# Performance work log

Measured on AMD Instinct MI355X. Metric: run time of the kernel, lower is better.

## Reference

```python
import math
import jax, jax.numpy as jnp
import numpy as np

Q_CLUSTER = 128
K_CLUSTER = 128


def _gaussian_orthogonal(m, d, rng):
    # gaussian_orthogonal_random_matrix with scaling=0 (row norms of fresh gaussians)
    blocks = []
    for _ in range(int(np.ceil(m / d))):
        g = rng.standard_normal((d, d))
        q, _ = np.linalg.qr(g)
        blocks.append(q.T)
    mat = np.concatenate(blocks, 0)[:m]
    norms = np.linalg.norm(rng.standard_normal((m, d)), axis=-1)
    return (mat * norms[:, None]).astype(np.float32)


def setup_inputs() -> dict:
    k = jax.random.key(0)
    kq, kk, kv = jax.random.split(k, 3)
    B, T, H, E = 2, 4096, 8, 64
    M, NH = 256, 4
    rng = np.random.default_rng(0)
    query = jax.random.normal(kq, (B, T, H, E), dtype=jnp.float32)
    key = jax.random.normal(kk, (B, T, H, E), dtype=jnp.float32)
    value = jax.random.normal(kv, (B, T, H, E), dtype=jnp.float32)
    proj = jnp.asarray(_gaussian_orthogonal(M, E, rng))
    alpha = jnp.asarray(rng.standard_normal((E + 2, NH)).astype(np.float32))
    beta = jnp.asarray(rng.uniform(0.0, 1.0, (1, NH)).astype(np.float32))
    return {"query": query, "key": key, "value": value, "proj": proj,
            "alpha": alpha, "beta": beta}


def _sort_to_buckets(x, perm, bucketsz):
    # x: (bh, s, d), perm: (nh, bh, s) -> (nh, bh, nbuckets, bucketsz, d)
    nh, bh, s = perm.shape
    g = jnp.take_along_axis(jnp.broadcast_to(x[None], (nh,) + x.shape),
                            perm[..., None], axis=2)
    return g.reshape(nh, bh, s // bucketsz, bucketsz, x.shape[-1])


def _unsort_from_buckets(s_x, perm_inv):
    nh, bh, nb, bsz, d = s_x.shape
    return jnp.take_along_axis(s_x.reshape(nh, bh, nb * bsz, d),
                               perm_inv[..., None], axis=2)


def _smyrf_forward(query, key, value, proj, alpha, beta):
    B, T, H, E = query.shape
    D = value.shape[-1]
    n_hashes = alpha.shape[-1]
    temp = 1.0 / math.sqrt(E)  # softmax_temp
    q = query.transpose(0, 2, 1, 3).reshape(B * H, T, E)
    k = key.transpose(0, 2, 1, 3).reshape(B * H, T, E)
    v = value.transpose(0, 2, 1, 3).reshape(B * H, T, D)

    # ---- XBOX+ asymmetric transform + E2LSH hashing (no grad path) ----
    qn = jnp.linalg.norm(q, axis=-1, keepdims=True)
    kn = jnp.linalg.norm(k, axis=-1, keepdims=True)
    MQ = jnp.max(qn, axis=1, keepdims=True)
    MK = jnp.max(kn, axis=1, keepdims=True)
    ext_q = jnp.sqrt(jnp.maximum(MQ ** 2 + MK ** 2 - qn ** 2, 0.0))
    ext_k = jnp.sqrt(jnp.maximum(MQ ** 2 + MK ** 2 - kn ** 2, 0.0))
    q_t = jnp.concatenate([q, ext_q, jnp.zeros_like(ext_q)], axis=-1)
    k_t = jnp.concatenate([k, jnp.zeros_like(ext_k), ext_k], axis=-1)
    q_hash = (q_t @ alpha + beta).transpose(2, 0, 1)  # (nh, bh, T)
    k_hash = (k_t @ alpha + beta).transpose(2, 0, 1)
    q_pos = jnp.argsort(q_hash, axis=-1)
    k_pos = jnp.argsort(k_hash, axis=-1)

    # ---- Performer (FAVOR+) softmax-kernel features with log scales ----
    dn = math.sqrt(temp)
    ratio = proj.shape[0] ** -0.5

    def feats(x, is_query):
        dash = jnp.einsum('bsd,md->bsm', dn * x, proj)
        diag = 0.5 * (dn ** 2) * jnp.sum(x * x, axis=-1, keepdims=True)
        logv = dash - diag
        if is_query:
            stab = jax.lax.stop_gradient(jnp.max(logv, axis=-1, keepdims=True))
        else:
            stab = jax.lax.stop_gradient(jnp.max(logv, axis=(-2, -1), keepdims=True))
        return jnp.exp(logv - stab) * ratio, stab

    q_prime, q_ls = feats(q, True)   # (bh, T, m), (bh, T, 1)
    k_prime, k_ls = feats(k, False)  # (bh, S, m), (bh, 1, 1)
    prime_log_scale = q_ls + k_ls    # (bh, T, 1)

    qk1 = jnp.einsum('btm,bm->bt', q_prime, k_prime.sum(axis=1))
    kv = jnp.einsum('bsm,bsd->bmd', k_prime, v)
    qkv = jnp.einsum('btm,bmd->btd', q_prime, kv)

    # ---- sort into LSH buckets, per-bucket attention ----
    s_q = _sort_to_buckets(q, q_pos, Q_CLUSTER)
    s_k = _sort_to_buckets(k, k_pos, K_CLUSTER)
    s_v = _sort_to_buckets(v, k_pos, K_CLUSTER)
    sq_p = _sort_to_buckets(q_prime, q_pos, Q_CLUSTER)
    sk_p = _sort_to_buckets(k_prime, k_pos, K_CLUSTER)
    s_pls = _sort_to_buckets(prime_log_scale, q_pos, Q_CLUSTER)

    inner = jnp.einsum('hbnie,hbnje->hbnij', s_q, s_k) * temp
    dots_prime = jnp.einsum('hbnim,hbnjm->hbnij', sq_p, sk_p)

    q_rev = jnp.argsort(q_pos, axis=-1)
    if n_hashes > 1:
        k_rev = jnp.argsort(k_pos, axis=-1)
        q_bidx = (q_rev // Q_CLUSTER).transpose(1, 2, 0)  # (bh, T, nh)
        k_bidx = (k_rev // K_CLUSTER).transpose(1, 2, 0)
        s_qb = _sort_to_buckets(q_bidx, q_pos, Q_CLUSTER)
        s_kb = _sort_to_buckets(k_bidx, k_pos, K_CLUSTER)
        dup = jnp.sum(s_qb[..., :, None, :] == s_kb[..., None, :, :],
                      axis=-1).astype(inner.dtype)
        inner = inner - jnp.log(dup)
        dots_prime = dots_prime / dup

    lse = jnp.maximum(jnp.max(inner, axis=-1, keepdims=True), s_pls)
    dots = jnp.exp(inner - lse) - dots_prime * jnp.exp(s_pls - lse)
    dots_sum = jnp.sum(dots, axis=-1, keepdims=True)
    so = jnp.einsum('hbnij,hbnjd->hbnid', dots, s_v)

    o = _unsort_from_buckets(so, q_rev)
    logits = _unsort_from_buckets(lse, q_rev)
    dots_sum_u = _unsort_from_buckets(dots_sum, q_rev)

    norm_ls = jax.nn.logsumexp(logits, axis=0)        # (bh, T, 1)
    probs = jnp.exp(logits - norm_ls[None])
    out_lsh = jnp.sum(o * probs, axis=0)
    prime_scale = jnp.exp(prime_log_scale - norm_ls)
    out = out_lsh + qkv * prime_scale
    normalization = jnp.sum(dots_sum_u * probs, axis=0) + qk1[..., None] * prime_scale
    out_n = out / jnp.maximum(normalization, 1e-6)
    return out_n.reshape(B, H, T, D).transpose(0, 2, 1, 3)


def reference(query, key, value, proj, alpha, beta):
    return _smyrf_forward(query, key, value, proj, alpha, beta)
```

## Files before the change

### kernel.cpp

```cpp
#include <hip/hip_runtime.h>
#include <stdint.h>
#include <math.h>

#define DEVI __device__ __forceinline__

constexpr int TB  = 2;
constexpr int TT  = 4096;
constexpr int TH  = 8;
constexpr int TE  = 64;
constexpr int TBH = 16;
constexpr int TM  = 256;
constexpr int TNH = 4;
constexpr float C_TEMP  = 0.125f;
constexpr float C_DN    = 0.35355339059327373f;
constexpr float C_RATIO = 0.0625f;

typedef __attribute__((ext_vector_type(8))) short bf16x8;
typedef __attribute__((ext_vector_type(4))) float f32x4;

constexpr size_t algn(size_t x){ return (x + 255) & ~(size_t)255; }
constexpr size_t OFF_QN2F = 0;
constexpr size_t OFF_KN2F = algn(OFF_QN2F + (size_t)TBH*TT*4);
constexpr size_t OFF_QN2D = algn(OFF_KN2F + (size_t)TBH*TT*4);
constexpr size_t OFF_KN2D = algn(OFF_QN2D + (size_t)TBH*TT*8);
constexpr size_t OFF_MQK2 = algn(OFF_KN2D + (size_t)TBH*TT*8);
constexpr size_t OFF_QMAXP= algn(OFF_MQK2 + (size_t)TBH*8);
constexpr size_t OFF_KMAXP= algn(OFF_QMAXP+ (size_t)TBH*16*8);
constexpr size_t OFF_QH   = algn(OFF_KMAXP+ (size_t)TBH*16*8);
constexpr size_t OFF_KH   = algn(OFF_QH   + (size_t)TNH*TBH*TT*8);
constexpr size_t OFF_QPOS = algn(OFF_KH   + (size_t)TNH*TBH*TT*8);
constexpr size_t OFF_KPOS = algn(OFF_QPOS + (size_t)TNH*TBH*TT*4);
constexpr size_t OFF_QREV = algn(OFF_KPOS + (size_t)TNH*TBH*TT*4);
constexpr size_t OFF_KREV = algn(OFF_QREV + (size_t)TNH*TBH*TT*4);
constexpr size_t OFF_KLSP = algn(OFF_KREV + (size_t)TNH*TBH*TT*4);
constexpr size_t OFF_KLS  = algn(OFF_KLSP + (size_t)TBH*128*4);
constexpr size_t OFF_QP   = algn(OFF_KLS  + (size_t)TBH*4);
constexpr size_t OFF_KP   = algn(OFF_QP   + (size_t)TBH*TT*TM*4);
constexpr size_t OFF_PLS  = algn(OFF_KP   + (size_t)TBH*TT*TM*4);
constexpr size_t OFF_KSUM = algn(OFF_PLS  + (size_t)TBH*TT*4);
constexpr size_t OFF_KV   = algn(OFF_KSUM + (size_t)TBH*TM*4);
constexpr size_t OFF_OT   = algn(OFF_KV   + (size_t)TBH*TM*TE*4);
constexpr size_t OFF_LSET = algn(OFF_OT   + (size_t)TNH*TBH*TT*TE*4);
constexpr size_t OFF_DSUM = algn(OFF_LSET + (size_t)TNH*TBH*TT*4);
constexpr size_t WS_NEED  = algn(OFF_DSUM + (size_t)TNH*TBH*TT*4);
constexpr size_t OFF_KVP  = OFF_QN2D;
constexpr size_t OFF_KSP  = OFF_KVP + (size_t)4*16*256*64*4;

DEVI float bf2f(uint32_t u16){ uint32_t x = u16 << 16; return __builtin_bit_cast(float, x); }
DEVI uint16_t f2bf(float f){
  uint32_t x = __builtin_bit_cast(uint32_t, f);
  uint32_t r = x + 0x7fffu + ((x >> 16) & 1u);
  return (uint16_t)(r >> 16);
}
DEVI int dupc(uint32_t x){
  return (int)((x & 0xffu) == 0) + (int)(((x >> 8) & 0xffu) == 0)
       + (int)(((x >> 16) & 0xffu) == 0) + (int)((x >> 24) == 0);
}
DEVI float lndup(int d){
  return d == 1 ? 0.f : d == 2 ? 0.69314718f : d == 3 ? 1.09861229f : 1.38629436f;
}
DEVI float rcpdup(int d){
  return d == 1 ? 1.f : d == 2 ? 0.5f : d == 3 ? 0.333333343f : 0.25f;
}

DEVI void stage64(char* rowp, const float4* src8, int hf){
  #pragma unroll
  for(int x = 0; x < 8; x++){
    float4 vv = src8[x];
    uint16_t hx = f2bf(vv.x), hy = f2bf(vv.y), hz = f2bf(vv.z), hw = f2bf(vv.w);
    float lx = vv.x - bf2f(hx), ly = vv.y - bf2f(hy), lz = vv.z - bf2f(hz), lw = vv.w - bf2f(hw);
    uint2 hp = make_uint2((uint32_t)hx | ((uint32_t)hy << 16), (uint32_t)hz | ((uint32_t)hw << 16));
    uint2 lp = make_uint2((uint32_t)f2bf(lx) | ((uint32_t)f2bf(ly) << 16),
                          (uint32_t)f2bf(lz) | ((uint32_t)f2bf(lw) << 16));
    *((uint2*)(rowp + 64*hf + 8*x)) = hp;
    *((uint2*)(rowp + 128 + 64*hf + 8*x)) = lp;
  }
}

__global__ void k_norms2(const float* __restrict__ q, const float* __restrict__ kk,
                         float* __restrict__ qn2f, float* __restrict__ kn2f,
                         double* __restrict__ qn2d, double* __restrict__ kn2d,
                         double* __restrict__ qmaxp, double* __restrict__ kmaxp){
  __shared__ double red[256];
  int bx = blockIdx.x; int chunk = bx & 15, bh = bx >> 4;
  int tid = threadIdx.x;
  int b = bh >> 3, hh = bh & 7;
  int t = chunk*256 + tid;
  const float4* r1 = (const float4*)(q + (((size_t)(b*TT + t)*TH) + hh)*TE);
  double s = 0.0;
  #pragma unroll
  for(int x = 0; x < 16; x++){
    float4 vv = r1[x];
    s += (double)vv.x*vv.x + (double)vv.y*vv.y + (double)vv.z*vv.z + (double)vv.w*vv.w;
  }
  qn2d[bh*TT + t] = s; qn2f[bh*TT + t] = (float)s;
  const float4* r2 = (const float4*)(kk + (((size_t)(b*TT + t)*TH) + hh)*TE);
  double s2 = 0.0;
  #pragma unroll
  for(int x = 0; x < 16; x++){
    float4 vv = r2[x];
    s2 += (double)vv.x*vv.x + (double)vv.y*vv.y + (double)vv.z*vv.z + (double)vv.w*vv.w;
  }
  kn2d[bh*TT + t] = s2; kn2f[bh*TT + t] = (float)s2;
  red[tid] = s; __syncthreads();
  for(int o = 128; o > 0; o >>= 1){ if(tid < o) red[tid] = fmax(red[tid], red[tid+o]); __syncthreads(); }
  if(tid == 0) qmaxp[bh*16 + chunk] = red[0];
  __syncthreads();
  red[tid] = s2; __syncthreads();
  for(int o = 128; o > 0; o >>= 1){ if(tid < o) red[tid] = fmax(red[tid], red[tid+o]); __syncthreads(); }
  if(tid == 0) kmaxp[bh*16 + chunk] = red[0];
}

__global__ void k_mqk(const double* __restrict__ qmaxp, const double* __restrict__ kmaxp,
                      double* __restrict__ mqk2){
  int bh = blockIdx.x;
  if(threadIdx.x == 0){
    double mq = -1e300, mk = -1e300;
    for(int i = 0; i < 16; i++){ mq = fmax(mq, qmaxp[bh*16 + i]); mk = fmax(mk, kmaxp[bh*16 + i]); }
    mqk2[bh] = mq + mk;
  }
}

__global__ void k_hash(const float* __restrict__ q, const float* __restrict__ kk,
                       const float* __restrict__ alpha, const float* __restrict__ beta,
                       const double* __restrict__ qn2d, const double* __restrict__ kn2d,
                       const double* __restrict__ mqk2,
                       double* __restrict__ qh, double* __restrict__ kh){
  __shared__ double al[264];
  __shared__ double be[4];
  int tid = threadIdx.x;
  for(int i = tid; i < 264; i += 256) al[i] = (double)alpha[i];
  if(tid < 4) be[tid] = (double)beta[tid];
  __syncthreads();
  int gid = blockIdx.x*256 + tid;
  int side = gid >> 16; int r = gid & 65535;
  int bh = r >> 12, t = r & 4095;
  int b = bh >> 3, hh = bh & 7;
  const float* x = (side ? kk : q) + (((size_t)(b*TT + t)*TH) + hh)*TE;
  const float4* xr = (const float4*)x;
  double a0 = 0.0, a1 = 0.0, a2 = 0.0, a3 = 0.0;
  #pragma unroll
  for(int c = 0; c < 16; c++){
    float4 vv = xr[c];
    const double* a = al + c*16;
    a0 += (double)vv.x*a[0]  + (double)vv.y*a[4]  + (double)vv.z*a[8]  + (double)vv.w*a[12];
    a1 += (double)vv.x*a[1]  + (double)vv.y*a[5]  + (double)vv.z*a[9]  + (double)vv.w*a[13];
    a2 += (double)vv.x*a[2]  + (double)vv.y*a[6]  + (double)vv.z*a[10] + (double)vv.w*a[14];
    a3 += (double)vv.x*a[3]  + (double)vv.y*a[7]  + (double)vv.z*a[11] + (double)vv.w*a[15];
  }
  double n2  = (side ? kn2d : qn2d)[bh*TT + t];
  double ext = sqrt(fmax(mqk2[bh] - n2, 0.0));
  int ec = side ? 65 : 64;
  double* dst = side ? kh : qh;
  dst[((size_t)0*TBH + bh)*TT + t] = a0 + ext*al[ec*4 + 0] + be[0];
  dst[((size_t)1*TBH + bh)*TT + t] = a1 + ext*al[ec*4 + 1] + be[1];
  dst[((size_t)2*TBH + bh)*TT + t] = a2 + ext*al[ec*4 + 2] + be[2];
  dst[((size_t)3*TBH + bh)*TT + t] = a3 + ext*al[ec*4 + 3] + be[3];
}

__global__ void k_sort(const double* __restrict__ qh, const double* __restrict__ kh,
                       int* __restrict__ qpos, int* __restrict__ kpos,
                       int* __restrict__ qrev, int* __restrict__ krev){
  __shared__ double v[4096];
  __shared__ int    ix[4096];
  int blk = blockIdx.x; int side = blk >> 6; int hb = blk & 63;
  const double* src = (side ? kh : qh) + (size_t)hb*TT;
  int tid = threadIdx.x;
  for(int i = tid; i < 4096; i += 1024){ v[i] = src[i]; ix[i] = i; }
  __syncthreads();
  for(int k = 2; k <= 4096; k <<= 1){
    for(int j = k >> 1; j > 0; j >>= 1){
      for(int i = tid; i < 4096; i += 1024){
        int l = i ^ j;
        if(l > i){
          double va = v[i], vb = v[l]; int ia = ix[i], ib = ix[l];
          bool gt  = (va > vb) || (va == vb && ia > ib);
          bool asc = ((i & k) == 0);
          if(gt == asc){ v[i] = vb; v[l] = va; ix[i] = ib; ix[l] = ia; }
        }
      }
      __syncthreads();
    }
  }
  int* pos = (side ? kpos : qpos) + (size_t)hb*TT;
  int* rev = (side ? krev : qrev) + (size_t)hb*TT;
  for(int i = tid; i < 4096; i += 1024){ int id = ix[i]; pos[i] = id; rev[id] = i; }
}

__launch_bounds__(512, 1)
__global__ void k_dash(const float* __restrict__ q, const float* __restrict__ kk,
                       const float* __restrict__ proj,
                       const float* __restrict__ qn2f, const float* __restrict__ kn2f,
                       float* __restrict__ qp, float* __restrict__ kdash,
                       float* __restrict__ klsp, float* __restrict__ pls){
  __shared__ __align__(16) float pjL[64*260];
  __shared__ __align__(16) float x_l[128*68];
  __shared__ float x_n[128];
  __shared__ float wred8[8];
  int tid = threadIdx.x;
  int bx = blockIdx.x;
  int side = bx >> 9; int r = bx & 511; int bh = r >> 5; int ch = r & 31;
  int b = bh >> 3, hh = bh & 7, t0 = ch*128;
  const float* x  = side ? kk   : q;
  const float* n2 = side ? kn2f : qn2f;

  #pragma unroll 8
  for(int it = 0; it < 32; it++){
    int idx = it*512 + tid;
    pjL[(idx & 63)*260 + (idx >> 6)] = proj[idx];
  }
  {
    int rr = tid >> 2, c = tid & 3;
    const float4* src = (const float4*)(x + (((size_t)(b*TT + t0 + rr)*TH) + hh)*TE);
    float4* dst = (float4*)(x_l + rr*68);
    #pragma unroll
    for(int i = 0; i < 4; i++) dst[c*4 + i] = src[c*4 + i];
  }
  if(tid < 128) x_n[tid] = n2[bh*TT + t0 + tid];
  __syncthreads();

  int ml = (tid & 15)*4;
  int tb = tid >> 4;
  float4 acc[4][4];
  #pragma unroll
  for(int tt = 0; tt < 4; tt++)
    #pragma unroll
    for(int g = 0; g < 4; g++) acc[tt][g] = make_float4(0.f,0.f,0.f,0.f);

  #pragma unroll 4
  for(int k4 = 0; k4 < 16; k4++){
    float4 xv[4];
    #pragma unroll
    for(int tt = 0; tt < 4; tt++)
      xv[tt] = *((const float4*)(x_l + (tb + 32*tt)*68 + k4*4));
    #pragma unroll
    for(int kk4 = 0; kk4 < 4; kk4++){
      int krow = k4*4 + kk4;
      #pragma unroll
      for(int g = 0; g < 4; g++){
        float4 pv = *((const float4*)(pjL + krow*260 + ml + 64*g));
        #pragma unroll
        for(int tt = 0; tt < 4; tt++){
          float xs = (kk4 == 0) ? xv[tt].x : (kk4 == 1) ? xv[tt].y : (kk4 == 2) ? xv[tt].z : xv[tt].w;
          acc[tt][g].x = fmaf(xs, pv.x, acc[tt][g].x);
          acc[tt][g].y = fmaf(xs, pv.y, acc[tt][g].y);
          acc[tt][g].z = fmaf(xs, pv.z, acc[tt][g].z);
          acc[tt][g].w = fmaf(xs, pv.w, acc[tt][g].w);
        }
      }
    }
  }

  if(side == 0){
    #pragma unroll
    for(int tt = 0; tt < 4; tt++){
      int t_r = tb + 32*tt;
      float diag = 0.5f*C_TEMP*x_n[t_r];
      float dd[4][4];
      float mx = -1e30f;
      #pragma unroll
      for(int g = 0; g < 4; g++){
        float4 a = acc[tt][g];
        dd[g][0] = fmaf(C_DN, a.x, -diag); dd[g][1] = fmaf(C_DN, a.y, -diag);
        dd[g][2] = fmaf(C_DN, a.z, -diag); dd[g][3] = fmaf(C_DN, a.w, -diag);
        mx = fmaxf(mx, fmaxf(fmaxf(dd[g][0], dd[g][1]), fmaxf(dd[g][2], dd[g][3])));
      }
      #pragma unroll
      for(int s = 1; s < 16; s <<= 1) mx = fmaxf(mx, __shfl_xor(mx, s, 64));
      size_t rowbase = ((size_t)bh*TT + t0 + t_r)*256;
      #pragma unroll
      for(int g = 0; g < 4; g++){
        float4 e;
        e.x = __expf(dd[g][0] - mx)*C_RATIO; e.y = __expf(dd[g][1] - mx)*C_RATIO;
        e.z = __expf(dd[g][2] - mx)*C_RATIO; e.w = __expf(dd[g][3] - mx)*C_RATIO;
        *((float4*)(qp + rowbase + ml + 64*g)) = e;
      }
      if((tid & 15) == 0) pls[(size_t)bh*TT + t0 + t_r] = mx;
    }
  } else {
    float mx = -1e30f;
    #pragma unroll
    for(int tt = 0; tt < 4; tt++){
      int t_r = tb + 32*tt;
      float diag = 0.5f*C_TEMP*x_n[t_r];
      size_t rowbase = ((size_t)bh*TT + t0 + t_r)*256;
      #pragma unroll
      for(int g = 0; g < 4; g++){
        float4 a = acc[tt][g];
        float4 dd;
        dd.x = fmaf(C_DN, a.x, -diag); dd.y = fmaf(C_DN, a.y, -diag);
        dd.z = fmaf(C_DN, a.z, -diag); dd.w = fmaf(C_DN, a.w, -diag);
        *((float4*)(kdash + rowbase + ml + 64*g)) = dd;
        mx = fmaxf(mx, fmaxf(fmaxf(dd.x, dd.y), fmaxf(dd.z, dd.w)));
      }
    }
    #pragma unroll
    for(int s = 32; s > 0; s >>= 1) mx = fmaxf(mx, __shfl_xor(mx, s, 64));
    if((tid & 63) == 0) wred8[tid >> 6] = mx;
    __syncthreads();
    if(tid == 0){
      float m = wred8[0];
      #pragma unroll
      for(int i = 1; i < 8; i++) m = fmaxf(m, wred8[i]);
      klsp[bh*32 + ch] = m;
    }
  }
}

__global__ void k_klsred(const float* __restrict__ klsp, float* __restrict__ kls){
  int bh = blockIdx.x, tid = threadIdx.x;
  float v = (tid < 32) ? klsp[bh*32 + tid] : -1e30f;
  #pragma unroll
  for(int o = 16; o > 0; o >>= 1) v = fmaxf(v, __shfl_xor(v, o, 64));
  if(tid == 0) kls[bh] = v;
}

__global__ void k_expk(float* __restrict__ kp, const float* __restrict__ kls){
  int tid = threadIdx.x; int blk = blockIdx.x;
  float4* p = (float4*)kp;
  size_t base = (size_t)blk*2048;
  float stab = kls[blk >> 7];
  #pragma unroll
  for(int i = 0; i < 8; i++){
    size_t ix = base + i*256 + tid;
    float4 vv = p[ix];
    vv.x = __expf(vv.x - stab)*C_RATIO; vv.y = __expf(vv.y - stab)*C_RATIO;
    vv.z = __expf(vv.z - stab)*C_RATIO; vv.w = __expf(vv.w - stab)*C_RATIO;
    p[ix] = vv;
  }
}

__global__ void k_kv2(const float* __restrict__ kp, const float* __restrict__ v,
                      float* __restrict__ kvp, float* __restrict__ ksump){
  int bx = blockIdx.x; int sc = bx >> 7; int rem = bx & 127; int bh = rem >> 3; int mt = rem & 7;
  int tid = threadIdx.x; int g = tid >> 6, d = tid & 63;
  int b = bh >> 3, hh = bh & 7; int m0 = mt*32;
  float a[8], sa[8];
  #pragma unroll
  for(int j = 0; j < 8; j++){ a[j] = 0.f; sa[j] = 0.f; }
  const float* kpb = kp + (size_t)bh*TT*256 + m0 + g;
  const float* vb  = v + (size_t)b*TT*TH*TE + hh*TE + d;
  int s0 = sc*1024;
  #pragma unroll 4
  for(int s = s0; s < s0 + 1024; s++){
    float vv = vb[(size_t)s*512];
    const float* kr = kpb + (size_t)s*256;
    #pragma unroll
    for(int j = 0; j < 8; j++){
      float kj = kr[4*j];
      a[j] = fmaf(kj, vv, a[j]); sa[j] += kj;
    }
  }
  #pragma unroll
  for(int j = 0; j < 8; j++){
    int m = m0 + g + 4*j;
    kvp[(((size_t)sc*16 + bh)*256 + m)*64 + d] = a[j];
    if(d == 0) ksump[((size_t)sc*16 + bh)*256 + m] = sa[j];
  }
}

__global__ void k_kvred(const float* __restrict__ kvp, const float* __restrict__ ksump,
                        float* __restrict__ kv, float* __restrict__ ksum){
  int bx = blockIdx.x, tid = threadIdx.x;
  if(bx < 256){
    size_t i = (size_t)bx*1024 + tid*4;
    float4 s = make_float4(0.f,0.f,0.f,0.f);
    #pragma unroll
    for(int sc = 0; sc < 4; sc++){
      float4 p = *((const float4*)(kvp + (size_t)sc*262144 + i));
      s.x += p.x; s.y += p.y; s.z += p.z; s.w += p.w;
    }
    *((float4*)(kv + i)) = s;
  } else {
    for(int m = tid; m < 4096; m += 256){
      float s = 0.f;
      #pragma unroll
      for(int sc = 0; sc < 4; sc++) s += ksump[sc*4096 + m];
      ksum[m] = s;
    }
  }
}

__launch_bounds__(256, 2)
__global__ void k_bucket(const float* __restrict__ q, const float* __restrict__ kk, const float* __restrict__ v,
                         const float* __restrict__ qp, const float* __restrict__ kp,
                         const int* __restrict__ qpos, const int* __restrict__ kpos,
                         const int* __restrict__ qrev, const int* __restrict__ krev,
                         const float* __restrict__ pls, const float* __restrict__ kls,
                         const float* __restrict__ qn2f, const float* __restrict__ kn2f,
                         float* __restrict__ o_t, float* __restrict__ lse_t, float* __restrict__ dsum_t){
  __shared__ __align__(16) char smem[73232];
  constexpr int OFS_B = 34816;
  int* qidxL   = (int*)(smem + 69632);
  int* kidxL   = (int*)(smem + 70144);
  int* qbpL    = (int*)(smem + 70656);
  int* kbpL    = (int*)(smem + 71168);
  float* lseL  = (float*)(smem + 71680);
  float* pfacL = (float*)(smem + 72192);
  float* kn2L  = (float*)(smem + 72704);
  float* kmaxP = (float*)(smem + 73216);

  int tid = threadIdx.x;
  int w = tid >> 6, lane = tid & 63, l15 = lane & 15, quad = lane >> 4;
  int bx = blockIdx.x; int n = bx & 31, bh = (bx >> 5) & 15, h = bx >> 9;
  int b = bh >> 3, hh = bh & 7;

  if(tid < 128){
    int tk = kpos[((size_t)h*TBH + bh)*TT + n*128 + tid];
    kidxL[tid] = tk;
    int pk = 0;
    #pragma unroll
    for(int h3 = 0; h3 < 4; h3++){ int rv = krev[((size_t)h3*TBH + bh)*TT + tk]; pk |= (rv >> 7) << (8*h3); }
    kbpL[tid] = pk;
    kn2L[tid] = kn2f[(size_t)bh*TT + tk];
    int tq = qpos[((size_t)h*TBH + bh)*TT + n*128 + tid];
    qidxL[tid] = tq;
    int pq = 0;
    #pragma unroll
    for(int h3 = 0; h3 < 4; h3++){ int rv = qrev[((size_t)h3*TBH + bh)*TT + tq]; pq |= (rv >> 7) << (8*h3); }
    qbpL[tid] = pq;
  }
  __syncthreads();
  if(tid < 64){
    float m = fmaxf(kn2L[tid], kn2L[tid + 64]);
    #pragma unroll
    for(int o = 32; o > 0; o >>= 1) m = fmaxf(m, __shfl_xor(m, o, 64));
    if(tid == 0) kmaxP[0] = m;
  }
  {
    int r = tid >> 1, hf = tid & 1;
    const float4* qs = (const float4*)(q  + (((size_t)(b*TT + qidxL[r])*TH) + hh)*TE) + hf*8;
    const float4* ks = (const float4*)(kk + (((size_t)(b*TT + kidxL[r])*TH) + hh)*TE) + hf*8;
    stage64(smem + r*272, qs, hf);
    stage64(smem + OFS_B + r*272, ks, hf);
  }
  __syncthreads();
  if(tid < 128){
    int tq = qidxL[tid];
    float plsv = pls[(size_t)bh*TT + tq] + kls[bh];
    float lse = fmaxf(plsv, C_TEMP * sqrtf(qn2f[(size_t)bh*TT + tq] * kmaxP[0]));
    lseL[tid] = lse;
    pfacL[tid] = __expf(plsv - lse);
  }

  f32x4 acc_s[2][8], acc_p[2][8];
  #pragma unroll
  for(int mt = 0; mt < 2; mt++)
    #pragma unroll
    for(int nt = 0; nt < 8; nt++){
      acc_s[mt][nt] = (f32x4){0.f,0.f,0.f,0.f};
      acc_p[mt][nt] = (f32x4){0.f,0.f,0.f,0.f};
    }

  {
    bf16x8 ahi[2][2], alo[2][2];
    #pragma unroll
    for(int mt = 0; mt < 2; mt++)
      #pragma unroll
      for(int ks = 0; ks < 2; ks++){
        const char* ap = smem + (32*w + 16*mt + l15)*272 + 64*ks + 16*quad;
        ahi[mt][ks] = *((const bf16x8*)ap);
        alo[mt][ks] = *((const bf16x8*)(ap + 128));
      }
    #pragma unroll
    for(int nt = 0; nt < 8; nt++){
      #pragma unroll
      for(int ks = 0; ks < 2; ks++){
        const char* bp = smem + OFS_B + (16*nt + l15)*272 + 64*ks + 16*quad;
        bf16x8 bhi = *((const bf16x8*)bp);
        bf16x8 blo = *((const bf16x8*)(bp + 128));
        #pragma unroll
        for(int mt = 0; mt < 2; mt++){
          acc_s[mt][nt] = __builtin_amdgcn_mfma_f32_16x16x32_bf16(ahi[mt][ks], bhi, acc_s[mt][nt], 0, 0, 0);
          acc_s[mt][nt] = __builtin_amdgcn_mfma_f32_16x16x32_bf16(ahi[mt][ks], blo, acc_s[mt][nt], 0, 0, 0);
          acc_s[mt][nt] = __builtin_amdgcn_mfma_f32_16x16x32_bf16(alo[mt][ks], bhi, acc_s[mt][nt], 0, 0, 0);
        }
      }
    }
  }
  __syncthreads();

  for(int c = 0; c < 4; c++){
    { int r = tid >> 1, hf = tid & 1;
      const float4* qs = (const float4*)(qp + ((size_t)bh*TT + qidxL[r])*256 + c*64) + hf*8;
      const float4* ks = (const float4*)(kp + ((size_t)bh*TT + kidxL[r])*256 + c*64) + hf*8;
      stage64(smem + r*272, qs, hf);
      stage64(smem + OFS_B + r*272, ks, hf);
    }
    __syncthreads();
    bf16x8 ahi[2][2], alo[2][2];
    #pragma unroll
    for(int mt = 0; mt < 2; mt++)
      #pragma unroll
      for(int ks = 0; ks < 2; ks++){
        const char* ap = smem + (32*w + 16*mt + l15)*272 + 64*ks + 16*quad;
        ahi[mt][ks] = *((const bf16x8*)ap);
        alo[mt][ks] = *((const bf16x8*)(ap + 128));
      }
    #pragma unroll
    for(int nt = 0; nt < 8; nt++){
      #pragma unroll
      for(int ks = 0; ks < 2; ks++){
        const char* bp = smem + OFS_B + (16*nt + l15)*272 + 64*ks + 16*quad;
        bf16x8 bhi = *((const bf16x8*)bp);
        bf16x8 blo = *((const bf16x8*)(bp + 128));
        #pragma unroll
        for(int mt = 0; mt < 2; mt++){
          acc_p[mt][nt] = __builtin_amdgcn_mfma_f32_16x16x32_bf16(ahi[mt][ks], bhi, acc_p[mt][nt], 0, 0, 0);
          acc_p[mt][nt] = __builtin_amdgcn_mfma_f32_16x16x32_bf16(ahi[mt][ks], blo, acc_p[mt][nt], 0, 0, 0);
          acc_p[mt][nt] = __builtin_amdgcn_mfma_f32_16x16x32_bf16(alo[mt][ks], bhi, acc_p[mt][nt], 0, 0, 0);
        }
      }
    }
    __syncthreads();
  }

  {
    int j = tid >> 1, hc = tid & 1;
    const float4* vs = (const float4*)(v + (((size_t)(b*TT + kidxL[j])*TH) + hh)*TE) + hc*8;
    #pragma unroll
    for(int x = 0; x < 8; x++){
      float4 vv = vs[x];
      int c0 = hc*32 + 4*x;
      float vals[4] = {vv.x, vv.y, vv.z, vv.w};
      #pragma unroll
      for(int i = 0; i < 4; i++){
        uint16_t hi = f2bf(vals[i]);
        float lo = vals[i] - bf2f(hi);
        *((uint16_t*)(smem + OFS_B + (c0 + i)*528 + 2*j)) = hi;
        *((uint16_t*)(smem + OFS_B + (c0 + i)*528 + 256 + 2*j)) = f2bf(lo);
      }
    }
  }
  int qbp_r[8]; float lse_r[8], pfac_r[8], dsump[8]; int kbp_c[8];
  #pragma unroll
  for(int i = 0; i < 8; i++){
    int r = 32*w + 16*(i >> 2) + 4*quad + (i & 3);
    qbp_r[i] = qbpL[r]; lse_r[i] = lseL[r]; pfac_r[i] = pfacL[r]; dsump[i] = 0.f;
  }
  #pragma unroll
  for(int nt = 0; nt < 8; nt++) kbp_c[nt] = kbpL[l15 + 16*nt];
  __syncthreads();

  f32x4 acc_o[2][4];
  #pragma unroll
  for(int mt = 0; mt < 2; mt++)
    #pragma unroll
    for(int nv = 0; nv < 4; nv++) acc_o[mt][nv] = (f32x4){0.f,0.f,0.f,0.f};

  #pragma unroll
  for(int hv = 0; hv < 2; hv++){
    #pragma unroll
    for(int nt = 0; nt < 4; nt++){
      int ntg = 4*hv + nt;
      #pragma unroll
      for(int mt = 0; mt < 2; mt++){
        f32x4 s4 = acc_s[mt][ntg], p4 = acc_p[mt][ntg];
        #pragma unroll
        for(int e = 0; e < 4; e++){
          int i = mt*4 + e;
          int du = dupc((uint32_t)(qbp_r[i] ^ kbp_c[ntg]));
          float ein  = __expf(fmaf(C_TEMP, s4[e], -lndup(du)) - lse_r[i]);
          float dots = fmaf(-p4[e]*rcpdup(du), pfac_r[i], ein);
          dsump[i] += dots;
          int row = 32*w + 16*mt + 4*quad + e;
          int colL = l15 + 16*nt;
          uint16_t hi = f2bf(dots);
          float lo = dots - bf2f(hi);
          *((uint16_t*)(smem + row*272 + 2*colL)) = hi;
          *((uint16_t*)(smem + row*272 + 128 + 2*colL)) = f2bf(lo);
        }
      }
    }
    bf16x8 dhi[2][2], dlo[2][2];
    #pragma unroll
    for(int mt = 0; mt < 2; mt++)
      #pragma unroll
      for(int ks = 0; ks < 2; ks++){
        const char* ap = smem + (32*w + 16*mt + l15)*272 + 64*ks + 16*quad;
        dhi[mt][ks] = *((const bf16x8*)ap);
        dlo[mt][ks] = *((const bf16x8*)(ap + 128));
      }
    #pragma unroll
    for(int nv = 0; nv < 4; nv++){
      #pragma unroll
      for(int ks = 0; ks < 2; ks++){
        const char* bp = smem + OFS_B + (16*nv + l15)*528 + 128*hv + 64*ks + 16*quad;
        bf16x8 vhi = *((const bf16x8*)bp);
        bf16x8 vlo = *((const bf16x8*)(bp + 256));
        #pragma unroll
        for(int mt = 0; mt < 2; mt++){
          acc_o[mt][nv] = __builtin_amdgcn_mfma_f32_16x16x32_bf16(dhi[mt][ks], vhi, acc_o[mt][nv], 0, 0, 0);
          acc_o[mt][nv] = __builtin_amdgcn_mfma_f32_16x16x32_bf16(dhi[mt][ks], vlo, acc_o[mt][nv], 0, 0, 0);
          acc_o[mt][nv] = __builtin_amdgcn_mfma_f32_16x16x32_bf16(dlo[mt][ks], vhi, acc_o[mt][nv], 0, 0, 0);
        }
      }
    }
  }

  #pragma unroll
  for(int i = 0; i < 8; i++){
    float s = dsump[i];
    s += __shfl_xor(s, 1, 64); s += __shfl_xor(s, 2, 64);
    s += __shfl_xor(s, 4, 64); s += __shfl_xor(s, 8, 64);
    dsump[i] = s;
  }
  size_t obase = ((size_t)h*TBH + bh)*TT;
  if(l15 == 0){
    #pragma unroll
    for(int i = 0; i < 8; i++){
      int r = 32*w + 16*(i >> 2) + 4*quad + (i & 3);
      int tq = qidxL[r];
      lse_t [obase + tq] = lse_r[i];
      dsum_t[obase + tq] = dsump[i];
    }
  }
  #pragma unroll
  for(int mt = 0; mt < 2; mt++){
    #pragma unroll
    for(int e = 0; e < 4; e++){
      int r = 32*w + 16*mt + 4*quad + e;
      int tq = qidxL[r];
      float* orow = o_t + (obase + tq)*64;
      #pragma unroll
      for(int nv = 0; nv < 4; nv++) orow[l15 + 16*nv] = acc_o[mt][nv][e];
    }
  }
}

__launch_bounds__(512, 1)
__global__ void k_final2(const float* __restrict__ qp, const float* __restrict__ kv,
                         const float* __restrict__ ksum, const float* __restrict__ o_t,
                         const float* __restrict__ lse_t, const float* __restrict__ dsum_t,
                         const float* __restrict__ pls, const float* __restrict__ kls,
                         float* __restrict__ out){
  __shared__ __align__(16) float kv_l[256*68];
  __shared__ __align__(16) float qp_l[128*68];
  __shared__ float prL[128][4];
  __shared__ float pscL[128];
  __shared__ float nrmL[128];
  int tid = threadIdx.x;
  int bx = blockIdx.x; int bh = bx >> 5, ch = bx & 31;
  int b = bh >> 3, hh = bh & 7;
  int t0 = ch*128;
  {
    const float4* kv4 = (const float4*)(kv + (size_t)bh*16384);
    #pragma unroll
    for(int i = 0; i < 8; i++){
      int idx = i*512 + tid;
      int m = idx >> 4, d4 = idx & 15;
      *((float4*)(kv_l + m*68 + d4*4)) = kv4[idx];
    }
    if(tid < 256) kv_l[tid*68 + 64] = ksum[bh*256 + tid];
  }
  int c = tid & 15, tb = tid >> 4;
  float4 acc[4];
  #pragma unroll
  for(int tt = 0; tt < 4; tt++) acc[tt] = make_float4(0.f,0.f,0.f,0.f);
  float p1 = 0.f;
  for(int c4 = 0; c4 < 4; c4++){
    __syncthreads();
    #pragma unroll
    for(int it = 0; it < 4; it++){
      int r = it*32 + tb;
      *((float4*)(qp_l + r*68 + c*4)) =
        *((const float4*)(qp + ((size_t)bh*TT + t0 + r)*256 + c4*64 + c*4));
    }
    __syncthreads();
    #pragma unroll 4
    for(int m4 = 0; m4 < 16; m4++){
      float4 qv[4];
      #pragma unroll
      for(int tt = 0; tt < 4; tt++)
        qv[tt] = *((const float4*)(qp_l + (tb + 32*tt)*68 + m4*4));
      #pragma unroll
      for(int mm = 0; mm < 4; mm++){
        int m = c4*64 + m4*4 + mm;
        float4 kvv = *((const float4*)(kv_l + m*68 + c*4));
        #pragma unroll
        for(int tt = 0; tt < 4; tt++){
          float qs = (mm == 0) ? qv[tt].x : (mm == 1) ? qv[tt].y : (mm == 2) ? qv[tt].z : qv[tt].w;
          acc[tt].x = fmaf(qs, kvv.x, acc[tt].x);
          acc[tt].y = fmaf(qs, kvv.y, acc[tt].y);
          acc[tt].z = fmaf(qs, kvv.z, acc[tt].z);
          acc[tt].w = fmaf(qs, kvv.w, acc[tt].w);
        }
      }
    }
    if(tid < 128){
      #pragma unroll 8
      for(int m = 0; m < 64; m++)
        p1 = fmaf(qp_l[tid*68 + m], kv_l[(c4*64 + m)*68 + 64], p1);
    }
  }
  __syncthreads();
  if(tid < 128){
    int t = t0 + tid;
    float l0 = lse_t[((size_t)0*TBH + bh)*TT + t], l1 = lse_t[((size_t)1*TBH + bh)*TT + t];
    float l2 = lse_t[((size_t)2*TBH + bh)*TT + t], l3 = lse_t[((size_t)3*TBH + bh)*TT + t];
    float M = fmaxf(fmaxf(l0, l1), fmaxf(l2, l3));
    float e0 = __expf(l0 - M), e1 = __expf(l1 - M), e2 = __expf(l2 - M), e3 = __expf(l3 - M);
    float rs = 1.f / (e0 + e1 + e2 + e3);
    float pr0 = e0*rs, pr1 = e1*rs, pr2 = e2*rs, pr3 = e3*rs;
    float psc = __expf(pls[bh*TT + t] + kls[bh] - M)*rs;
    float nrm = 0.f;
    nrm = fmaf(dsum_t[((size_t)0*TBH + bh)*TT + t], pr0, nrm);
    nrm = fmaf(dsum_t[((size_t)1*TBH + bh)*TT + t], pr1, nrm);
    nrm = fmaf(dsum_t[((size_t)2*TBH + bh)*TT + t], pr2, nrm);
    nrm = fmaf(dsum_t[((size_t)3*TBH + bh)*TT + t], pr3, nrm);
    nrm = fmaf(p1, psc, nrm);
    prL[tid][0] = pr0; prL[tid][1] = pr1; prL[tid][2] = pr2; prL[tid][3] = pr3;
    pscL[tid] = psc;
    nrmL[tid] = fmaxf(nrm, 1e-6f);
  }
  __syncthreads();
  #pragma unroll
  for(int tt = 0; tt < 4; tt++){
    int r = tb + 32*tt; int t = t0 + r;
    float4 o0 = *((const float4*)(o_t + (((size_t)0*TBH + bh)*TT + t)*64 + c*4));
    float4 o1 = *((const float4*)(o_t + (((size_t)1*TBH + bh)*TT + t)*64 + c*4));
    float4 o2 = *((const float4*)(o_t + (((size_t)2*TBH + bh)*TT + t)*64 + c*4));
    float4 o3 = *((const float4*)(o_t + (((size_t)3*TBH + bh)*TT + t)*64 + c*4));
    float pr0 = prL[r][0], pr1 = prL[r][1], pr2 = prL[r][2], pr3 = prL[r][3];
    float psc = pscL[r], nrm = nrmL[r];
    float4 outl;
    outl.x = fmaf(o3.x, pr3, fmaf(o2.x, pr2, fmaf(o1.x, pr1, o0.x*pr0)));
    outl.y = fmaf(o3.y, pr3, fmaf(o2.y, pr2, fmaf(o1.y, pr1, o0.y*pr0)));
    outl.z = fmaf(o3.z, pr3, fmaf(o2.z, pr2, fmaf(o1.z, pr1, o0.z*pr0)));
    outl.w = fmaf(o3.w, pr3, fmaf(o2.w, pr2, fmaf(o1.w, pr1, o0.w*pr0)));
    float4 res;
    res.x = (outl.x + acc[tt].x*psc) / nrm;
    res.y = (outl.y + acc[tt].y*psc) / nrm;
    res.z = (outl.z + acc[tt].z*psc) / nrm;
    res.w = (outl.w + acc[tt].w*psc) / nrm;
    *((float4*)(out + ((size_t)(b*TT + t)*TH + hh)*64 + c*4)) = res;
  }
}

__global__ void k_sentinel(float* __restrict__ out, int n){
  int i = blockIdx.x*256 + threadIdx.x;
  if(i < n) out[i] = 12345.0f;
}

extern "C" void kernel_launch(void* const* d_in, const int* in_sizes, int n_in,
                              void* d_out, int out_size, void* d_ws, size_t ws_size,
                              hipStream_t stream){
  const float* q     = (const float*)d_in[0];
  const float* k     = (const float*)d_in[1];
  const float* v     = (const float*)d_in[2];
  const float* proj  = (const float*)d_in[3];
  const float* alpha = (const float*)d_in[4];
  const float* beta  = (const float*)d_in[5];
  float* out = (float*)d_out;
  char* ws = (char*)d_ws;

  if(ws_size < WS_NEED){
    k_sentinel<<<dim3((out_size + 255)/256), dim3(256), 0, stream>>>(out, out_size);
    return;
  }

  float*  qn2f  = (float*) (ws + OFF_QN2F);
  float*  kn2f  = (float*) (ws + OFF_KN2F);
  double* qn2d  = (double*)(ws + OFF_QN2D);
  double* kn2d  = (double*)(ws + OFF_KN2D);
  double* mqk2  = (double*)(ws + OFF_MQK2);
  double* qmaxp = (double*)(ws + OFF_QMAXP);
  double* kmaxp = (double*)(ws + OFF_KMAXP);
  double* qh    = (double*)(ws + OFF_QH);
  double* kh    = (double*)(ws + OFF_KH);
  int*   qpos   = (int*)  (ws + OFF_QPOS);
  int*   kpos   = (int*)  (ws + OFF_KPOS);
  int*   qrev   = (int*)  (ws + OFF_QREV);
  int*   krev   = (int*)  (ws + OFF_KREV);
  float* klsp   = (float*)(ws + OFF_KLSP);
  float* kls    = (float*)(ws + OFF_KLS);
  float* qp     = (float*)(ws + OFF_QP);
  float* kp     = (float*)(ws + OFF_KP);
  float* pls    = (float*)(ws + OFF_PLS);
  float* ksum   = (float*)(ws + OFF_KSUM);
  float* kvv    = (float*)(ws + OFF_KV);
  float* o_t    = (float*)(ws + OFF_OT);
  float* lse_t  = (float*)(ws + OFF_LSET);
  float* dsum_t = (float*)(ws + OFF_DSUM);
  float* kvp    = (float*)(ws + OFF_KVP);
  float* ksump  = (float*)(ws + OFF_KSP);

  k_norms2<<<dim3(256),   dim3(256),  0, stream>>>(q, k, qn2f, kn2f, qn2d, kn2d, qmaxp, kmaxp);
  k_mqk   <<<dim3(16),    dim3(64),   0, stream>>>(qmaxp, kmaxp, mqk2);
  k_hash  <<<dim3(512),   dim3(256),  0, stream>>>(q, k, alpha, beta, qn2d, kn2d, mqk2, qh, kh);
  k_sort  <<<dim3(128),   dim3(1024), 0, stream>>>(qh, kh, qpos, kpos, qrev, krev);
  k_dash  <<<dim3(1024),  dim3(512),  0, stream>>>(q, k, proj, qn2f, kn2f, qp, kp, klsp, pls);
  k_klsred<<<dim3(16),    dim3(64),   0, stream>>>(klsp, kls);
  k_expk  <<<dim3(2048),  dim3(256),  0, stream>>>(kp, kls);
  k_kv2   <<<dim3(512),   dim3(256),  0, stream>>>(kp, v, kvp, ksump);
  k_kvred <<<dim3(257),   dim3(256),  0, stream>>>(kvp, ksump, kvv, ksum);
  k_bucket<<<dim3(2048),  dim3(256),  0, stream>>>(q, k, v, qp, kp, qpos, kpos, qrev, krev, pls, kls, qn2f, kn2f, o_t, lse_t, dsum_t);
  k_final2<<<dim3(512),   dim3(512),  0, stream>>>(qp, kvv, ksum, o_t, lse_t, dsum_t, pls, kls, out);
}
```

Before: 805.2 us.

## Use split-bf16 MFMA in k_dash, vectorize k_kv2 loads, prefetch bucket staging

k_dash replaces its scalar fp32 FMA projection with three-term hi/lo bf16 MFMA products, staging x and proj in shared memory at 256 threads per block. k_kv2 reassigns features so each thread reads two contiguous float4s per row instead of eight strided scalars. k_bucket prefetches the next 64-column chunk of qp/kp (and finally v) into registers while the current MFMAs run, hiding gather latency. The split-bf16 path adds a small precision change and more register pressure.

New measurement: 777.0 us. 1.04x faster.

```diff
diff --git a/kernel.cpp b/kernel.cpp
--- a/kernel.cpp
+++ b/kernel.cpp
@@ -76,6 +76,19 @@
     *((uint2*)(rowp + 128 + 64*hf + 8*x)) = lp;
   }
 }
+DEVI void stage64r(char* rowp, const float4* vv8, int hf){
+  #pragma unroll
+  for(int x = 0; x < 8; x++){
+    float4 vv = vv8[x];
+    uint16_t hx = f2bf(vv.x), hy = f2bf(vv.y), hz = f2bf(vv.z), hw = f2bf(vv.w);
+    float lx = vv.x - bf2f(hx), ly = vv.y - bf2f(hy), lz = vv.z - bf2f(hz), lw = vv.w - bf2f(hw);
+    uint2 hp = make_uint2((uint32_t)hx | ((uint32_t)hy << 16), (uint32_t)hz | ((uint32_t)hw << 16));
+    uint2 lp = make_uint2((uint32_t)f2bf(lx) | ((uint32_t)f2bf(ly) << 16),
+                          (uint32_t)f2bf(lz) | ((uint32_t)f2bf(lw) << 16));
+    *((uint2*)(rowp + 64*hf + 8*x)) = hp;
+    *((uint2*)(rowp + 128 + 64*hf + 8*x)) = lp;
+  }
+}
 
 __global__ void k_norms2(const float* __restrict__ q, const float* __restrict__ kk,
                          float* __restrict__ qn2f, float* __restrict__ kn2f,
@@ -187,123 +200,113 @@
   for(int i = tid; i < 4096; i += 1024){ int id = ix[i]; pos[i] = id; rev[id] = i; }
 }
 
-__launch_bounds__(512, 1)
+__launch_bounds__(256, 1)
 __global__ void k_dash(const float* __restrict__ q, const float* __restrict__ kk,
                        const float* __restrict__ proj,
                        const float* __restrict__ qn2f, const float* __restrict__ kn2f,
                        float* __restrict__ qp, float* __restrict__ kdash,
                        float* __restrict__ klsp, float* __restrict__ pls){
-  __shared__ __align__(16) float pjL[64*260];
-  __shared__ __align__(16) float x_l[128*68];
+  __shared__ __align__(16) char xb[128*272];
+  __shared__ __align__(16) char pb[256*272];
   __shared__ float x_n[128];
-  __shared__ float wred8[8];
+  __shared__ float wred4[4];
   int tid = threadIdx.x;
+  int w = tid >> 6, lane = tid & 63, l15 = lane & 15, quad = lane >> 4;
   int bx = blockIdx.x;
-  int side = bx >> 9; int r = bx & 511; int bh = r >> 5; int ch = r & 31;
+  int side = bx >> 9; int r0 = bx & 511; int bh = r0 >> 5; int ch = r0 & 31;
   int b = bh >> 3, hh = bh & 7, t0 = ch*128;
   const float* x  = side ? kk   : q;
   const float* n2 = side ? kn2f : qn2f;
 
-  #pragma unroll 8
-  for(int it = 0; it < 32; it++){
-    int idx = it*512 + tid;
-    pjL[(idx & 63)*260 + (idx >> 6)] = proj[idx];
-  }
-  {
-    int rr = tid >> 2, c = tid & 3;
-    const float4* src = (const float4*)(x + (((size_t)(b*TT + t0 + rr)*TH) + hh)*TE);
-    float4* dst = (float4*)(x_l + rr*68);
-    #pragma unroll
-    for(int i = 0; i < 4; i++) dst[c*4 + i] = src[c*4 + i];
+  { int r = tid >> 1, hf = tid & 1;
+    const float4* src = (const float4*)(x + (((size_t)(b*TT + t0 + r)*TH) + hh)*TE) + hf*8;
+    stage64(xb + r*272, src, hf); }
+  #pragma unroll
+  for(int p = 0; p < 2; p++){
+    int r = p*128 + (tid >> 1); int hf = tid & 1;
+    const float4* src = (const float4*)(proj + (size_t)r*64) + hf*8;
+    stage64(pb + r*272, src, hf);
   }
   if(tid < 128) x_n[tid] = n2[bh*TT + t0 + tid];
   __syncthreads();
 
-  int ml = (tid & 15)*4;
-  int tb = tid >> 4;
-  float4 acc[4][4];
-  #pragma unroll
-  for(int tt = 0; tt < 4; tt++)
-    #pragma unroll
-    for(int g = 0; g < 4; g++) acc[tt][g] = make_float4(0.f,0.f,0.f,0.f);
-
+  f32x4 acc[2][16];
+  #pragma unroll
+  for(int tt = 0; tt < 2; tt++)
+    #pragma unroll
+    for(int nt = 0; nt < 16; nt++) acc[tt][nt] = (f32x4){0.f,0.f,0.f,0.f};
+
+  bf16x8 ahi[2][2], alo[2][2];
+  #pragma unroll
+  for(int tt = 0; tt < 2; tt++)
+    #pragma unroll
+    for(int ks = 0; ks < 2; ks++){
+      const char* ap = xb + (32*w + 16*tt + l15)*272 + 64*ks + 16*quad;
+      ahi[tt][ks] = *((const bf16x8*)ap);
+      alo[tt][ks] = *((const bf16x8*)(ap + 128));
+    }
   #pragma unroll 4
-  for(int k4 = 0; k4 < 16; k4++){
-    float4 xv[4];
-    #pragma unroll
-    for(int tt = 0; tt < 4; tt++)
-      xv[tt] = *((const float4*)(x_l + (tb + 32*tt)*68 + k4*4));
-    #pragma unroll
-    for(int kk4 = 0; kk4 < 4; kk4++){
-      int krow = k4*4 + kk4;
-      #pragma unroll
-      for(int g = 0; g < 4; g++){
-        float4 pv = *((const float4*)(pjL + krow*260 + ml + 64*g));
+  for(int nt = 0; nt < 16; nt++){
+    #pragma unroll
+    for(int ks = 0; ks < 2; ks++){
+      const char* bp = pb + (16*nt + l15)*272 + 64*ks + 16*quad;
+      bf16x8 bhi = *((const bf16x8*)bp);
+      bf16x8 blo = *((const bf16x8*)(bp + 128));
+      #pragma unroll
+      for(int tt = 0; tt < 2; tt++){
+        acc[tt][nt] = __builtin_amdgcn_mfma_f32_16x16x32_bf16(ahi[tt][ks], bhi, acc[tt][nt], 0, 0, 0);
+        acc[tt][nt] = __builtin_amdgcn_mfma_f32_16x16x32_bf16(ahi[tt][ks], blo, acc[tt][nt], 0, 0, 0);
+        acc[tt][nt] = __builtin_amdgcn_mfma_f32_16x16x32_bf16(alo[tt][ks], bhi, acc[tt][nt], 0, 0, 0);
+      }
+    }
+  }
+
+  if(side == 0){
+    #pragma unroll
+    for(int tt = 0; tt < 2; tt++){
+      #pragma unroll
+      for(int e = 0; e < 4; e++){
+        int t_r = 32*w + 16*tt + 4*quad + e;
+        float diag = 0.5f*C_TEMP*x_n[t_r];
+        float dv[16];
+        float mx = -1e30f;
         #pragma unroll
-        for(int tt = 0; tt < 4; tt++){
-          float xs = (kk4 == 0) ? xv[tt].x : (kk4 == 1) ? xv[tt].y : (kk4 == 2) ? xv[tt].z : xv[tt].w;
-          acc[tt][g].x = fmaf(xs, pv.x, acc[tt][g].x);
-          acc[tt][g].y = fmaf(xs, pv.y, acc[tt][g].y);
-          acc[tt][g].z = fmaf(xs, pv.z, acc[tt][g].z);
-          acc[tt][g].w = fmaf(xs, pv.w, acc[tt][g].w);
+        for(int nt = 0; nt < 16; nt++){
+          dv[nt] = fmaf(C_DN, acc[tt][nt][e], -diag);
+          mx = fmaxf(mx, dv[nt]);
         }
-      }
-    }
-  }
-
-  if(side == 0){
-    #pragma unroll
-    for(int tt = 0; tt < 4; tt++){
-      int t_r = tb + 32*tt;
-      float diag = 0.5f*C_TEMP*x_n[t_r];
-      float dd[4][4];
-      float mx = -1e30f;
-      #pragma unroll
-      for(int g = 0; g < 4; g++){
-        float4 a = acc[tt][g];
-        dd[g][0] = fmaf(C_DN, a.x, -diag); dd[g][1] = fmaf(C_DN, a.y, -diag);
-        dd[g][2] = fmaf(C_DN, a.z, -diag); dd[g][3] = fmaf(C_DN, a.w, -diag);
-        mx = fmaxf(mx, fmaxf(fmaxf(dd[g][0], dd[g][1]), fmaxf(dd[g][2], dd[g][3])));
-      }
-      #pragma unroll
-      for(int s = 1; s < 16; s <<= 1) mx = fmaxf(mx, __shfl_xor(mx, s, 64));
-      size_t rowbase = ((size_t)bh*TT + t0 + t_r)*256;
-      #pragma unroll
-      for(int g = 0; g < 4; g++){
-        float4 e;
-        e.x = __expf(dd[g][0] - mx)*C_RATIO; e.y = __expf(dd[g][1] - mx)*C_RATIO;
-        e.z = __expf(dd[g][2] - mx)*C_RATIO; e.w = __expf(dd[g][3] - mx)*C_RATIO;
-        *((float4*)(qp + rowbase + ml + 64*g)) = e;
-      }
-      if((tid & 15) == 0) pls[(size_t)bh*TT + t0 + t_r] = mx;
+        #pragma unroll
+        for(int s = 1; s < 16; s <<= 1) mx = fmaxf(mx, __shfl_xor(mx, s, 64));
+        size_t rowbase = ((size_t)bh*TT + t0 + t_r)*256;
+        #pragma unroll
+        for(int nt = 0; nt < 16; nt++)
+          qp[rowbase + l15 + 16*nt] = __expf(dv[nt] - mx)*C_RATIO;
+        if(l15 == 0) pls[(size_t)bh*TT + t0 + t_r] = mx;
+      }
     }
   } else {
     float mx = -1e30f;
     #pragma unroll
-    for(int tt = 0; tt < 4; tt++){
-      int t_r = tb + 32*tt;
-      float diag = 0.5f*C_TEMP*x_n[t_r];
-      size_t rowbase = ((size_t)bh*TT + t0 + t_r)*256;
-      #pragma unroll
-      for(int g = 0; g < 4; g++){
-        float4 a = acc[tt][g];
-        float4 dd;
-        dd.x = fmaf(C_DN, a.x, -diag); dd.y = fmaf(C_DN, a.y, -diag);
-        dd.z = fmaf(C_DN, a.z, -diag); dd.w = fmaf(C_DN, a.w, -diag);
-        *((float4*)(kdash + rowbase + ml + 64*g)) = dd;
-        mx = fmaxf(mx, fmaxf(fmaxf(dd.x, dd.y), fmaxf(dd.z, dd.w)));
+    for(int tt = 0; tt < 2; tt++){
+      #pragma unroll
+      for(int e = 0; e < 4; e++){
+        int t_r = 32*w + 16*tt + 4*quad + e;
+        float diag = 0.5f*C_TEMP*x_n[t_r];
+        size_t rowbase = ((size_t)bh*TT + t0 + t_r)*256;
+        #pragma unroll
+        for(int nt = 0; nt < 16; nt++){
+          float d = fmaf(C_DN, acc[tt][nt][e], -diag);
+          kdash[rowbase + l15 + 16*nt] = d;
+          mx = fmaxf(mx, d);
+        }
       }
     }
     #pragma unroll
     for(int s = 32; s > 0; s >>= 1) mx = fmaxf(mx, __shfl_xor(mx, s, 64));
-    if((tid & 63) == 0) wred8[tid >> 6] = mx;
+    if(lane == 0) wred4[w] = mx;
     __syncthreads();
-    if(tid == 0){
-      float m = wred8[0];
-      #pragma unroll
-      for(int i = 1; i < 8; i++) m = fmaxf(m, wred8[i]);
-      klsp[bh*32 + ch] = m;
-    }
+    if(tid == 0)
+      klsp[bh*32 + ch] = fmaxf(fmaxf(wred4[0], wred4[1]), fmaxf(wred4[2], wred4[3]));
   }
 }
 
@@ -334,26 +337,26 @@
                       float* __restrict__ kvp, float* __restrict__ ksump){
   int bx = blockIdx.x; int sc = bx >> 7; int rem = bx & 127; int bh = rem >> 3; int mt = rem & 7;
   int tid = threadIdx.x; int g = tid >> 6, d = tid & 63;
-  int b = bh >> 3, hh = bh & 7; int m0 = mt*32;
+  int b = bh >> 3, hh = bh & 7;
+  int mbase = mt*32 + 8*g;
   float a[8], sa[8];
   #pragma unroll
   for(int j = 0; j < 8; j++){ a[j] = 0.f; sa[j] = 0.f; }
-  const float* kpb = kp + (size_t)bh*TT*256 + m0 + g;
+  const float* kpb = kp + (size_t)bh*TT*256 + mbase;
   const float* vb  = v + (size_t)b*TT*TH*TE + hh*TE + d;
   int s0 = sc*1024;
   #pragma unroll 4
   for(int s = s0; s < s0 + 1024; s++){
     float vv = vb[(size_t)s*512];
-    const float* kr = kpb + (size_t)s*256;
-    #pragma unroll
-    for(int j = 0; j < 8; j++){
-      float kj = kr[4*j];
-      a[j] = fmaf(kj, vv, a[j]); sa[j] += kj;
-    }
+    const float4* kr = (const float4*)(kpb + (size_t)s*256);
+    float4 k0 = kr[0], k1 = kr[1];
+    float f[8] = {k0.x, k0.y, k0.z, k0.w, k1.x, k1.y, k1.z, k1.w};
+    #pragma unroll
+    for(int j = 0; j < 8; j++){ a[j] = fmaf(f[j], vv, a[j]); sa[j] += f[j]; }
   }
   #pragma unroll
   for(int j = 0; j < 8; j++){
-    int m = m0 + g + 4*j;
+    int m = mbase + j;
     kvp[(((size_t)sc*16 + bh)*256 + m)*64 + d] = a[j];
     if(d == 0) ksump[((size_t)sc*16 + bh)*256 + m] = sa[j];
   }
@@ -443,6 +446,14 @@
     pfacL[tid] = __expf(plsv - lse);
   }
 
+  float4 pq[8], pk2[8];
+  { int r = tid >> 1, hf = tid & 1;
+    const float4* qs = (const float4*)(qp + ((size_t)bh*TT + qidxL[r])*256) + hf*8;
+    const float4* ks = (const float4*)(kp + ((size_t)bh*TT + kidxL[r])*256) + hf*8;
+    #pragma unroll
+    for(int i = 0; i < 8; i++){ pq[i] = qs[i]; pk2[i] = ks[i]; }
+  }
+
   f32x4 acc_s[2][8], acc_p[2][8];
   #pragma unroll
   for(int mt = 0; mt < 2; mt++)
@@ -482,12 +493,22 @@
 
   for(int c = 0; c < 4; c++){
     { int r = tid >> 1, hf = tid & 1;
-      const float4* qs = (const float4*)(qp + ((size_t)bh*TT + qidxL[r])*256 + c*64) + hf*8;
-      const float4* ks = (const float4*)(kp + ((size_t)bh*TT + kidxL[r])*256 + c*64) + hf*8;
-      stage64(smem + r*272, qs, hf);
-      stage64(smem + OFS_B + r*272, ks, hf);
+      stage64r(smem + r*272, pq, hf);
+      stage64r(smem + OFS_B + r*272, pk2, hf);
     }
     __syncthreads();
+    if(c < 3){
+      int r = tid >> 1, hf = tid & 1;
+      const float4* qs = (const float4*)(qp + ((size_t)bh*TT + qidxL[r])*256 + (c+1)*64) + hf*8;
+      const float4* ks = (const float4*)(kp + ((size_t)bh*TT + kidxL[r])*256 + (c+1)*64) + hf*8;
+      #pragma unroll
+      for(int i = 0; i < 8; i++){ pq[i] = qs[i]; pk2[i] = ks[i]; }
+    } else {
+      int j = tid >> 1, hc = tid & 1;
+      const float4* vs = (const float4*)(v + (((size_t)(b*TT + kidxL[j])*TH) + hh)*TE) + hc*8;
+      #pragma unroll
+      for(int i = 0; i < 8; i++) pq[i] = vs[i];
+    }
     bf16x8 ahi[2][2], alo[2][2];
     #pragma unroll
     for(int mt = 0; mt < 2; mt++)
@@ -517,10 +538,9 @@
 
   {
     int j = tid >> 1, hc = tid & 1;
-    const float4* vs = (const float4*)(v + (((size_t)(b*TT + kidxL[j])*TH) + hh)*TE) + hc*8;
     #pragma unroll
     for(int x = 0; x < 8; x++){
-      float4 vv = vs[x];
+      float4 vv = pq[x];
       int c0 = hc*32 + 4*x;
       float vals[4] = {vv.x, vv.y, vv.z, vv.w};
       #pragma unroll
@@ -789,7 +809,7 @@
   k_mqk   <<<dim3(16),    dim3(64),   0, stream>>>(qmaxp, kmaxp, mqk2);
   k_hash  <<<dim3(512),   dim3(256),  0, stream>>>(q, k, alpha, beta, qn2d, kn2d, mqk2, qh, kh);
   k_sort  <<<dim3(128),   dim3(1024), 0, stream>>>(qh, kh, qpos, kpos, qrev, krev);
-  k_dash  <<<dim3(1024),  dim3(512),  0, stream>>>(q, k, proj, qn2f, kn2f, qp, kp, klsp, pls);
+  k_dash  <<<dim3(1024),  dim3(256),  0, stream>>>(q, k, proj, qn2f, kn2f, qp, kp, klsp, pls);
   k_klsred<<<dim3(16),    dim3(64),   0, stream>>>(klsp, kls);
   k_expk  <<<dim3(2048),  dim3(256),  0, stream>>>(kp, kls);
   k_kv2   <<<dim3(512),   dim3(256),  0, stream>>>(kp, v, kvp, ksump);
```
